# Optimization experiments

Measured on AMD Instinct MI355X. Metric: run time of the kernel, lower is better.

Reference implementation:

```python
import jax, jax.numpy as jnp
import numpy as np

PAD = 0

def setup_inputs() -> dict:
    key = jax.random.key(0)
    ks = jax.random.split(key, 16)
    B, S, D, F = 64, 512, 768, 256
    VOCAB = 32000
    # variable-length tweets: length in [8, S], rest is padding (token id PAD=0)
    lengths = jax.random.randint(ks[0], (B,), 8, S + 1)
    tok = jax.random.randint(ks[1], (B, S), 1, VOCAB)
    x = jnp.where(jnp.arange(S)[None, :] < lengths[:, None], tok, PAD)
    h = jax.random.normal(ks[2], (B, S, D), dtype=jnp.float32)
    sc = 0.02
    w2 = jax.random.normal(ks[3], (F, D, 2), dtype=jnp.float32) * sc
    b2 = jax.random.normal(ks[4], (F,), dtype=jnp.float32) * sc
    w3 = jax.random.normal(ks[5], (F, D, 3), dtype=jnp.float32) * sc
    b3 = jax.random.normal(ks[6], (F,), dtype=jnp.float32) * sc
    w4 = jax.random.normal(ks[7], (F, D, 4), dtype=jnp.float32) * sc
    b4 = jax.random.normal(ks[8], (F,), dtype=jnp.float32) * sc
    w5 = jax.random.normal(ks[9], (F, D, 5), dtype=jnp.float32) * sc
    b5 = jax.random.normal(ks[10], (F,), dtype=jnp.float32) * sc
    fc_w = jax.random.normal(ks[11], (1, 4 * F), dtype=jnp.float32) * sc
    fc_b = jax.random.normal(ks[12], (1,), dtype=jnp.float32) * sc
    return {"x": x, "h": h, "w2": w2, "b2": b2, "w3": w3, "b3": b3,
            "w4": w4, "b4": b4, "w5": w5, "b5": b5, "fc_w": fc_w, "fc_b": fc_b}


def _branch(hc, L, w, b):
    # hc: [B, D, S] front-compacted hidden states; w: [F, D, k]
    k = w.shape[-1]
    out = jax.lax.conv_general_dilated(
        hc, w, window_strides=(1,), padding='VALID',
        dimension_numbers=('NCH', 'OIH', 'NCH')) + b[None, :, None]  # [B,F,S-k+1]
    T = out.shape[-1]
    # conv position t is valid iff t + k - 1 < L  <=>  t < L - k + 1
    valid = jnp.arange(T)[None, :] < (L - k + 1)[:, None]           # [B,T]
    neg = jnp.asarray(-jnp.inf, out.dtype)
    pooled = jnp.max(jnp.where(valid[:, None, :], out, neg), axis=-1)  # [B,F]
    return jax.nn.relu(pooled)


def reference(x, h, w2, b2, w3, b3, w4, b4, w5, b5, fc_w, fc_b):
    mask = x != PAD                                   # [B,S]
    L = mask.sum(axis=1)                              # [B]
    # stable compaction: move non-pad token hidden states to the front, order preserved
    order = jnp.argsort(jnp.logical_not(mask), axis=1, stable=True)   # [B,S]
    hc = jnp.take_along_axis(h, order[..., None], axis=1)             # [B,S,D]
    hc = hc.transpose(0, 2, 1)                                        # [B,D,S]
    feats = jnp.concatenate([
        _branch(hc, L, w2, b2),
        _branch(hc, L, w3, b3),
        _branch(hc, L, w4, b4),
        _branch(hc, L, w5, b5),
    ], axis=-1)                                       # [B, 4F]
    logits = feats @ fc_w.T + fc_b                    # [B,1]
    return jax.nn.sigmoid(logits).squeeze(-1)         # [B]
```

## Files before the change

### kernel.cpp

```cpp
#include <hip/hip_runtime.h>
#include <stdint.h>

#define Bn 64
#define Sn 512
#define SPn 520
#define Dn 768
#define JSTRIDE 196608
#define ABUF 16640
#define BSLOT 8192
#define QS_A 28.222222f
#define SAQ 0.035433072f

typedef int iv4 __attribute__((ext_vector_type(4)));

static __device__ __forceinline__ signed char q8(float f, float s) {
  float t = __builtin_rintf(f * s);
  t = fmaxf(-127.f, fminf(127.f, t));
  return (signed char)(int)t;
}

static __device__ __forceinline__ void gload16(const void* g, void* l) {
  __builtin_amdgcn_global_load_lds(
      (const __attribute__((address_space(1))) unsigned int*)g,
      (__attribute__((address_space(3))) unsigned int*)l, 16, 0, 0);
}

template<int N> __device__ __forceinline__ void waitv() {
  static_assert(N == 0 || N == 2 || N == 7, "");
  if constexpr (N == 0) asm volatile("s_waitcnt vmcnt(0)" ::: "memory");
  else if constexpr (N == 2) asm volatile("s_waitcnt vmcnt(2)" ::: "memory");
  else asm volatile("s_waitcnt vmcnt(7)" ::: "memory");
}

__global__ __launch_bounds__(256) void compact_kernel(
    const int* __restrict__ x, const float* __restrict__ h,
    signed char* __restrict__ hcq, int* __restrict__ Lout) {
  int b = blockIdx.x, rblk = blockIdx.y;
  __shared__ unsigned long long masks[8];
  __shared__ short sidx[Sn];
  int tid = threadIdx.x, lane = tid & 63, wv = tid >> 6;
  for (int c = wv; c < 8; c += 4) {
    bool pred = x[b * Sn + c * 64 + lane] != 0;
    unsigned long long m = __ballot(pred);
    if (lane == 0) masks[c] = m;
  }
  __syncthreads();
  int pref[9]; pref[0] = 0;
  #pragma unroll
  for (int c = 0; c < 8; ++c) pref[c + 1] = pref[c] + __popcll(masks[c]);
  int L = pref[8];
  for (int p = tid; p < Sn; p += 256) {
    int c = p >> 6, l = p & 63;
    unsigned long long m = masks[c];
    if ((m >> l) & 1ull)
      sidx[pref[c] + __popcll(m & ((1ull << l) - 1ull))] = (short)p;
  }
  if (rblk == 0 && tid == 0) Lout[b] = L;
  __syncthreads();
  int r0 = rblk * 65;
  for (int r = r0 + wv; r < r0 + 65; r += 4) {
    if (r < L) {
      signed char* dst = hcq + ((size_t)b * SPn + r) * Dn;
      const float* src = h + ((size_t)b * Sn + sidx[r]) * Dn;
      #pragma unroll
      for (int c = 0; c < 3; ++c) {
        int d = c * 256 + lane * 4;
        float4 v = *(const float4*)(src + d);
        char4 o = { q8(v.x, QS_A), q8(v.y, QS_A), q8(v.z, QS_A), q8(v.w, QS_A) };
        *(char4*)(dst + d) = o;
      }
    }
  }
}

__global__ __launch_bounds__(256) void plan_kernel(
    const int* __restrict__ Lbuf, int* __restrict__ plan, int* __restrict__ rowmap) {
  __shared__ int sOff[65];
  __shared__ int sL[64];
  int tid = threadIdx.x;
  if (tid < 64) {
    int L = Lbuf[tid];
    int SL = (L + 15) & ~15;
    int pre = SL;
    #pragma unroll
    for (int off = 1; off < 64; off <<= 1) {
      int y = __shfl_up(pre, off);
      if (tid >= off) pre += y;
    }
    sOff[tid] = pre - SL;
    sL[tid] = L;
    if (tid == 63) { sOff[64] = pre; plan[0] = (pre + 255) >> 8; }
  }
  __syncthreads();
  int M = sOff[64];
  for (int b = 0; b < 64; ++b) {
    int off = sOff[b], L = sL[b];
    int SL = (L + 15) & ~15;
    int enc = (b << 20) | (L << 10);
    for (int t = tid; t < SL; t += 256) rowmap[off + t] = enc | t;
  }
  for (int p = M + tid; p < M + 264; p += 256)
    rowmap[p] = 512;
}

__global__ __launch_bounds__(256) void wpack_kernel(
    const float* __restrict__ w2, const float* __restrict__ w3,
    const float* __restrict__ w4, const float* __restrict__ w5,
    signed char* __restrict__ wq, float* __restrict__ fscale) {
  __shared__ float sf[3840];
  __shared__ float smax[4];
  int bb = blockIdx.x;
  int br = bb >> 8, f = bb & 255, k = br + 2;
  const float* w = (br == 0) ? w2 : (br == 1) ? w3 : (br == 2) ? w4 : w5;
  int mBase = 256 * ((br * (br + 3)) >> 1);
  const float* src = w + (size_t)f * Dn * k;
  int n = Dn * k;
  int tid = threadIdx.x, lane = tid & 63, wv = tid >> 6;
  float mx = 0.f;
  for (int e = tid; e < n; e += 256) {
    float v = src[e];
    sf[e] = v;
    mx = fmaxf(mx, fabsf(v));
  }
  #pragma unroll
  for (int off = 32; off; off >>= 1) mx = fmaxf(mx, __shfl_xor(mx, off));
  if (lane == 0) smax[wv] = mx;
  __syncthreads();
  float M = fmaxf(fmaxf(smax[0], smax[1]), fmaxf(smax[2], smax[3]));
  M = fmaxf(M, 1e-30f);
  if (tid == 0) fscale[br * 256 + f] = M / 127.f;
  float qs = 127.f / M;
  for (int j = 0; j < k; ++j) {
    signed char* dst = wq + (size_t)(mBase + j * 256 + f) * Dn;
    for (int d = tid; d < Dn; d += 256) dst[d] = q8(sf[d * k + j], qs);
  }
}

static __device__ __forceinline__ void issueA(
    int d0i, char* sA, const char* const (&gA)[4], const char* gAt,
    int lane, int wvoff) {
  int aoff = (d0i + 1) * 64;
  char* nA = sA + ((d0i + 1) & 1) * ABUF;
  #pragma unroll
  for (int p = 0; p < 4; ++p) gload16(gA[p] + aoff, nA + p * 4096 + wvoff);
  if (lane < 16) gload16(gAt + aoff, nA + 16384);
}

template<int J, int W, int J2, int DADD, int DOA>
static __device__ __forceinline__ void conv_step(
    int d0i, int bsl0, char* sA, char* sB,
    const char* const (&gA)[4], const char* gAt, const char* gB0,
    int lane, int wv, int lrow, int lg, int wvoff, iv4 (&acc)[4][8]) {
  int sl = bsl0 + J;      sl  -= (sl  >= 3) ? 3 : 0; sl  -= (sl  >= 3) ? 3 : 0;
  int dsl = bsl0 + J + 2; dsl -= (dsl >= 3) ? 3 : 0; dsl -= (dsl >= 3) ? 3 : 0; dsl -= (dsl >= 3) ? 3 : 0;
  {
    int boff = J2 * JSTRIDE + (d0i + DADD) * 64;
    char* bdst = sB + dsl * BSLOT + wvoff;
    gload16(gB0 + boff, bdst);
    gload16(gB0 + 49152 + boff, bdst + 4096);
  }
  if constexpr (DOA) issueA(d0i, sA, gA, gAt, lane, wvoff);
  const char* curA = sA + (d0i & 1) * ABUF;
  const char* curB = sB + sl * BSLOT;
  iv4 Af[4], Bf[8];
  #pragma unroll
  for (int m = 0; m < 4; ++m) {
    int row = wv * 64 + m * 16 + lrow + J;
    Af[m] = *(const iv4*)(curA + row * 64 + ((lg ^ ((row >> 1) & 3)) << 4));
  }
  #pragma unroll
  for (int n = 0; n < 8; ++n) {
    int row = n * 16 + lrow;
    Bf[n] = *(const iv4*)(curB + row * 64 + ((lg ^ ((row >> 1) & 3)) << 4));
  }
  __builtin_amdgcn_s_setprio(1);
  #pragma unroll
  for (int n = 0; n < 8; ++n)
    #pragma unroll
    for (int m = 0; m < 4; ++m)
      acc[m][n] = __builtin_amdgcn_mfma_i32_16x16x64_i8(Af[m], Bf[n], acc[m][n], 0, 0, 0);
  __builtin_amdgcn_s_setprio(0);
  __builtin_amdgcn_sched_barrier(0);
  waitv<W>();
  __builtin_amdgcn_sched_barrier(0);
  __builtin_amdgcn_s_barrier();
  __builtin_amdgcn_sched_barrier(0);
}

#define SA bsl0, sA, sB, gA, gAt, gB0, lane, wv, lrow, lg, wvoff, acc

template<int KK>
static __device__ __forceinline__ void conv_loop(
    char* sA, char* sB, const char* const (&gA)[4], const char* gAt,
    const char* gB0,
    int lane, int wv, int lrow, int lg, int wvoff, iv4 (&acc)[4][8]) {
  #pragma unroll
  for (int p = 0; p < 4; ++p) gload16(gA[p], sA + p * 4096 + wvoff);
  if (lane < 16) gload16(gAt, sA + 16384);
  gload16(gB0, sB + wvoff);
  gload16(gB0 + 49152, sB + 4096 + wvoff);
  gload16(gB0 + JSTRIDE, sB + BSLOT + wvoff);
  gload16(gB0 + 49152 + JSTRIDE, sB + BSLOT + 4096 + wvoff);
  __builtin_amdgcn_sched_barrier(0);
  waitv<2>();
  __builtin_amdgcn_sched_barrier(0);
  __builtin_amdgcn_s_barrier();
  __builtin_amdgcn_sched_barrier(0);
  int bsl0 = 0;
  for (int d0i = 0; d0i < 11; ++d0i) {
    if constexpr (KK == 5) {
      conv_step<0,7,2,0,1>(d0i, SA);
      conv_step<1,7,3,0,0>(d0i, SA);
      conv_step<2,2,4,0,0>(d0i, SA);
      conv_step<3,2,0,1,0>(d0i, SA);
      conv_step<4,2,1,1,0>(d0i, SA);
    } else if constexpr (KK == 4) {
      conv_step<0,7,2,0,1>(d0i, SA);
      conv_step<1,7,3,0,0>(d0i, SA);
      conv_step<2,2,0,1,0>(d0i, SA);
      conv_step<3,2,1,1,0>(d0i, SA);
    } else if constexpr (KK == 3) {
      conv_step<0,7,2,0,1>(d0i, SA);
      conv_step<1,7,0,1,0>(d0i, SA);
      conv_step<2,2,1,1,0>(d0i, SA);
    } else {
      conv_step<0,7,0,1,1>(d0i, SA);
      conv_step<1,2,1,1,0>(d0i, SA);
    }
    bsl0 += KK; bsl0 -= (bsl0 >= 3) ? 3 : 0; bsl0 -= (bsl0 >= 3) ? 3 : 0;
  }
  if constexpr (KK == 5) {
    conv_step<0,2,2,0,0>(11, SA);
    conv_step<1,2,3,0,0>(11, SA);
    conv_step<2,2,4,0,0>(11, SA);
    conv_step<3,2,0,1,0>(11, SA);
    conv_step<4,2,1,1,0>(11, SA);
  } else if constexpr (KK == 4) {
    conv_step<0,2,2,0,0>(11, SA);
    conv_step<1,2,3,0,0>(11, SA);
    conv_step<2,2,0,1,0>(11, SA);
    conv_step<3,2,1,1,0>(11, SA);
  } else if constexpr (KK == 3) {
    conv_step<0,2,2,0,0>(11, SA);
    conv_step<1,2,0,1,0>(11, SA);
    conv_step<2,2,1,1,0>(11, SA);
  } else {
    conv_step<0,2,0,1,0>(11, SA);
    conv_step<1,2,1,1,0>(11, SA);
  }
  waitv<0>();
}

__global__ __launch_bounds__(256, 2) void conv_kernel(
    const signed char* __restrict__ hcq, const signed char* __restrict__ wq,
    const float* __restrict__ b2, const float* __restrict__ b3,
    const float* __restrict__ b4, const float* __restrict__ b5,
    const float* __restrict__ fscale,
    const int* __restrict__ plan, const int* __restrict__ rowmap,
    int* __restrict__ feats) {
  __shared__ char smem[2 * ABUF + 3 * BSLOT];
  char* sA = smem;
  char* sB = smem + 2 * ABUF;
  int idx = blockIdx.x;
  int xcd = idx & 7, s2 = idx >> 3;
  int sub = s2 & 7, tile = xcd + ((s2 >> 3) << 3);
  if (tile >= plan[0]) return;
  int br = 3 - (sub >> 1), ff = sub & 1, kk = br + 2;
  int mBase = 256 * ((br * (br + 3)) >> 1) + ff * 128;
  const float* bias = (br == 0) ? b2 : (br == 1) ? b3 : (br == 2) ? b4 : b5;
  int tid = threadIdx.x, lane = tid & 63, wv = tid >> 6;
  int lrow = lane & 15, lg = lane >> 4;
  int wvoff = wv * 1024;
  int P0 = tile << 8;

  const char* gA[4];
  #pragma unroll
  for (int p = 0; p < 4; ++p) {
    int c = p * 256 + tid;
    int row = c >> 2, sgp = c & 3;
    int rm = rowmap[P0 + row];
    int bb_ = rm >> 20, t = rm & 1023;
    int seg = sgp ^ ((row >> 1) & 3);
    gA[p] = (const char*)(hcq + ((size_t)(bb_ * SPn + t)) * Dn + seg * 16);
  }
  const char* gAt;
  {
    int l = lane & 15;
    int row = 256 + (l >> 2), sgp = l & 3;
    int rm = rowmap[P0 + row];
    int bb_ = rm >> 20, t = rm & 1023;
    int seg = sgp ^ ((row >> 1) & 3);
    gAt = (const char*)(hcq + ((size_t)(bb_ * SPn + t)) * Dn + seg * 16);
  }
  const char* gB0;
  {
    int row = tid >> 2, sgp = tid & 3;
    int seg = sgp ^ ((row >> 1) & 3);
    gB0 = (const char*)(wq + ((size_t)(mBase + row)) * Dn + seg * 16);
  }

  iv4 acc[4][8];
  #pragma unroll
  for (int m = 0; m < 4; ++m)
    #pragma unroll
    for (int n = 0; n < 8; ++n) acc[m][n] = (iv4)0;

  switch (br) {
    case 3: conv_loop<5>(sA, sB, gA, gAt, gB0, lane, wv, lrow, lg, wvoff, acc); break;
    case 2: conv_loop<4>(sA, sB, gA, gAt, gB0, lane, wv, lrow, lg, wvoff, acc); break;
    case 1: conv_loop<3>(sA, sB, gA, gAt, gB0, lane, wv, lrow, lg, wvoff, acc); break;
    default: conv_loop<2>(sA, sB, gA, gAt, gB0, lane, wv, lrow, lg, wvoff, acc); break;
  }

  int rmv[4];
  #pragma unroll
  for (int m = 0; m < 4; ++m) rmv[m] = rowmap[P0 + wv * 64 + m * 16];
  #pragma unroll
  for (int n = 0; n < 8; ++n) {
    int fg = ff * 128 + n * 16 + lrow;
    float bv = bias[fg];
    float sfc = fscale[br * 256 + fg] * SAQ;
    #pragma unroll
    for (int m = 0; m < 4; ++m) {
      int bb_ = rmv[m] >> 20;
      int Lb = (rmv[m] >> 10) & 1023;
      int t0 = (rmv[m] & 1023) + lg * 4;
      int vlim = Lb - kk + 1;
      float pmax = 0.f;
      #pragma unroll
      for (int i = 0; i < 4; ++i) {
        float v = (float)acc[m][n][i] * sfc + bv;
        pmax = fmaxf(pmax, (t0 + i < vlim) ? fmaxf(v, 0.f) : 0.f);
      }
      pmax = fmaxf(pmax, __shfl_xor(pmax, 16));
      pmax = fmaxf(pmax, __shfl_xor(pmax, 32));
      if (lane < 16 && pmax > 0.f)
        atomicMax(feats + bb_ * 1024 + br * 256 + fg, __float_as_int(pmax));
    }
  }
}

__global__ __launch_bounds__(64) void fc_kernel(
    const int* __restrict__ feats, const float* __restrict__ fcw,
    const float* __restrict__ fcb, float* __restrict__ out) {
  int b = blockIdx.x, lane = threadIdx.x;
  float acc = 0.f;
  for (int i = lane; i < 1024; i += 64)
    acc += __int_as_float(feats[b * 1024 + i]) * fcw[i];
  #pragma unroll
  for (int off = 32; off; off >>= 1) acc += __shfl_xor(acc, off);
  if (lane == 0) out[b] = 1.f / (1.f + expf(-(acc + fcb[0])));
}

extern "C" void kernel_launch(void* const* d_in, const int* in_sizes, int n_in,
                              void* d_out, int out_size, void* d_ws, size_t ws_size,
                              hipStream_t stream) {
  const int*   x   = (const int*)d_in[0];
  const float* h   = (const float*)d_in[1];
  const float* w2  = (const float*)d_in[2];
  const float* b2  = (const float*)d_in[3];
  const float* w3  = (const float*)d_in[4];
  const float* b3  = (const float*)d_in[5];
  const float* w4  = (const float*)d_in[6];
  const float* b4  = (const float*)d_in[7];
  const float* w5  = (const float*)d_in[8];
  const float* b5  = (const float*)d_in[9];
  const float* fcw = (const float*)d_in[10];
  const float* fcb = (const float*)d_in[11];
  float* out = (float*)d_out;
  char* ws = (char*)d_ws;
  signed char* hcq = (signed char*)ws;
  signed char* wq  = (signed char*)(ws + 25559040);
  float* fscale = (float*)(ws + 28311552);
  int* feats  = (int*)(ws + 28315648);
  int* Lbuf   = (int*)(ws + 28577792);
  int* plan   = (int*)(ws + 28578048);
  int* rowmap = (int*)(ws + 28578064);

  hipMemsetAsync(feats, 0, 64 * 1024 * 4, stream);
  compact_kernel<<<dim3(64, 8), 256, 0, stream>>>(x, h, hcq, Lbuf);
  plan_kernel<<<1, 256, 0, stream>>>(Lbuf, plan, rowmap);
  wpack_kernel<<<1024, 256, 0, stream>>>(w2, w3, w4, w5, wq, fscale);
  conv_kernel<<<1024, 256, 0, stream>>>(hcq, wq, b2, b3, b4, b5, fscale, plan, rowmap, feats);
  fc_kernel<<<64, 64, 0, stream>>>(feats, fcw, fcb, out);
}
```

Before: 115.8 us.

## Fuse compaction and weight packing into one launch; split conv tile over 8 waves

Merges the compaction and weight-quantization kernels into a single stage kernel with 1536 blocks. The plan kernel now computes lengths directly from the token ids, so it no longer depends on compaction. The conv kernel moves from 4 waves with 64x128 per-wave tiles to 8 waves in a 4x2 grid with 64x64 per-wave tiles. This halves accumulator registers and global loads per thread, and the launch bounds are raised to target more occupancy. The cost is more LDS fragment reads per MFMA and barriers shared across more waves.

```diff
diff --git a/kernel.cpp b/kernel.cpp
--- a/kernel.cpp
+++ b/kernel.cpp
@@ -26,60 +26,28 @@
 }
 
 template<int N> __device__ __forceinline__ void waitv() {
-  static_assert(N == 0 || N == 2 || N == 7, "");
+  static_assert(N == 0 || N == 1 || N == 4, "");
   if constexpr (N == 0) asm volatile("s_waitcnt vmcnt(0)" ::: "memory");
-  else if constexpr (N == 2) asm volatile("s_waitcnt vmcnt(2)" ::: "memory");
-  else asm volatile("s_waitcnt vmcnt(7)" ::: "memory");
-}
-
-__global__ __launch_bounds__(256) void compact_kernel(
-    const int* __restrict__ x, const float* __restrict__ h,
-    signed char* __restrict__ hcq, int* __restrict__ Lout) {
-  int b = blockIdx.x, rblk = blockIdx.y;
-  __shared__ unsigned long long masks[8];
-  __shared__ short sidx[Sn];
+  else if constexpr (N == 1) asm volatile("s_waitcnt vmcnt(1)" ::: "memory");
+  else asm volatile("s_waitcnt vmcnt(4)" ::: "memory");
+}
+
+__global__ __launch_bounds__(256) void plan_kernel(
+    const int* __restrict__ x, int* __restrict__ plan, int* __restrict__ rowmap) {
+  __shared__ int sL[64];
+  __shared__ int sOff[65];
   int tid = threadIdx.x, lane = tid & 63, wv = tid >> 6;
-  for (int c = wv; c < 8; c += 4) {
-    bool pred = x[b * Sn + c * 64 + lane] != 0;
-    unsigned long long m = __ballot(pred);
-    if (lane == 0) masks[c] = m;
+  for (int bb = wv; bb < 64; bb += 4) {
+    int cnt = 0;
+    for (int c = 0; c < 8; ++c) {
+      unsigned long long m = __ballot(x[bb * Sn + c * 64 + lane] != 0);
+      cnt += __popcll(m);
+    }
+    if (lane == 0) sL[bb] = cnt;
   }
   __syncthreads();
-  int pref[9]; pref[0] = 0;
-  #pragma unroll
-  for (int c = 0; c < 8; ++c) pref[c + 1] = pref[c] + __popcll(masks[c]);
-  int L = pref[8];
-  for (int p = tid; p < Sn; p += 256) {
-    int c = p >> 6, l = p & 63;
-    unsigned long long m = masks[c];
-    if ((m >> l) & 1ull)
-      sidx[pref[c] + __popcll(m & ((1ull << l) - 1ull))] = (short)p;
-  }
-  if (rblk == 0 && tid == 0) Lout[b] = L;
-  __syncthreads();
-  int r0 = rblk * 65;
-  for (int r = r0 + wv; r < r0 + 65; r += 4) {
-    if (r < L) {
-      signed char* dst = hcq + ((size_t)b * SPn + r) * Dn;
-      const float* src = h + ((size_t)b * Sn + sidx[r]) * Dn;
-      #pragma unroll
-      for (int c = 0; c < 3; ++c) {
-        int d = c * 256 + lane * 4;
-        float4 v = *(const float4*)(src + d);
-        char4 o = { q8(v.x, QS_A), q8(v.y, QS_A), q8(v.z, QS_A), q8(v.w, QS_A) };
-        *(char4*)(dst + d) = o;
-      }
-    }
-  }
-}
-
-__global__ __launch_bounds__(256) void plan_kernel(
-    const int* __restrict__ Lbuf, int* __restrict__ plan, int* __restrict__ rowmap) {
-  __shared__ int sOff[65];
-  __shared__ int sL[64];
-  int tid = threadIdx.x;
   if (tid < 64) {
-    int L = Lbuf[tid];
+    int L = sL[tid];
     int SL = (L + 15) & ~15;
     int pre = SL;
     #pragma unroll
@@ -88,7 +56,6 @@
       if (tid >= off) pre += y;
     }
     sOff[tid] = pre - SL;
-    sL[tid] = L;
     if (tid == 63) { sOff[64] = pre; plan[0] = (pre + 255) >> 8; }
   }
   __syncthreads();
@@ -103,79 +70,116 @@
     rowmap[p] = 512;
 }
 
-__global__ __launch_bounds__(256) void wpack_kernel(
+__global__ __launch_bounds__(256) void stage_kernel(
+    const int* __restrict__ x, const float* __restrict__ h,
     const float* __restrict__ w2, const float* __restrict__ w3,
     const float* __restrict__ w4, const float* __restrict__ w5,
-    signed char* __restrict__ wq, float* __restrict__ fscale) {
-  __shared__ float sf[3840];
-  __shared__ float smax[4];
-  int bb = blockIdx.x;
-  int br = bb >> 8, f = bb & 255, k = br + 2;
-  const float* w = (br == 0) ? w2 : (br == 1) ? w3 : (br == 2) ? w4 : w5;
-  int mBase = 256 * ((br * (br + 3)) >> 1);
-  const float* src = w + (size_t)f * Dn * k;
-  int n = Dn * k;
+    signed char* __restrict__ hcq, signed char* __restrict__ wq,
+    float* __restrict__ fscale) {
   int tid = threadIdx.x, lane = tid & 63, wv = tid >> 6;
-  float mx = 0.f;
-  for (int e = tid; e < n; e += 256) {
-    float v = src[e];
-    sf[e] = v;
-    mx = fmaxf(mx, fabsf(v));
-  }
-  #pragma unroll
-  for (int off = 32; off; off >>= 1) mx = fmaxf(mx, __shfl_xor(mx, off));
-  if (lane == 0) smax[wv] = mx;
-  __syncthreads();
-  float M = fmaxf(fmaxf(smax[0], smax[1]), fmaxf(smax[2], smax[3]));
-  M = fmaxf(M, 1e-30f);
-  if (tid == 0) fscale[br * 256 + f] = M / 127.f;
-  float qs = 127.f / M;
-  for (int j = 0; j < k; ++j) {
-    signed char* dst = wq + (size_t)(mBase + j * 256 + f) * Dn;
-    for (int d = tid; d < Dn; d += 256) dst[d] = q8(sf[d * k + j], qs);
+  if (blockIdx.x < 512) {
+    int cidx = blockIdx.x;
+    int b = cidx >> 3, rblk = cidx & 7;
+    __shared__ unsigned long long masks[8];
+    __shared__ short sidx[Sn];
+    for (int c = wv; c < 8; c += 4) {
+      unsigned long long m = __ballot(x[b * Sn + c * 64 + lane] != 0);
+      if (lane == 0) masks[c] = m;
+    }
+    __syncthreads();
+    int pref[9]; pref[0] = 0;
+    #pragma unroll
+    for (int c = 0; c < 8; ++c) pref[c + 1] = pref[c] + __popcll(masks[c]);
+    int L = pref[8];
+    for (int p = tid; p < Sn; p += 256) {
+      int c = p >> 6, l = p & 63;
+      unsigned long long m = masks[c];
+      if ((m >> l) & 1ull)
+        sidx[pref[c] + __popcll(m & ((1ull << l) - 1ull))] = (short)p;
+    }
+    __syncthreads();
+    int r0 = rblk * 65;
+    for (int r = r0 + wv; r < r0 + 65; r += 4) {
+      if (r < L) {
+        signed char* dst = hcq + ((size_t)b * SPn + r) * Dn;
+        const float* src = h + ((size_t)b * Sn + sidx[r]) * Dn;
+        #pragma unroll
+        for (int c = 0; c < 3; ++c) {
+          int d = c * 256 + lane * 4;
+          float4 v = *(const float4*)(src + d);
+          char4 o = { q8(v.x, QS_A), q8(v.y, QS_A), q8(v.z, QS_A), q8(v.w, QS_A) };
+          *(char4*)(dst + d) = o;
+        }
+      }
+    }
+  } else {
+    __shared__ float sf[3840];
+    __shared__ float smax[4];
+    int bb = blockIdx.x - 512;
+    int br = bb >> 8, f = bb & 255, k = br + 2;
+    const float* w = (br == 0) ? w2 : (br == 1) ? w3 : (br == 2) ? w4 : w5;
+    int mBase = 256 * ((br * (br + 3)) >> 1);
+    const float* src = w + (size_t)f * Dn * k;
+    int n = Dn * k;
+    float mx = 0.f;
+    for (int e = tid; e < n; e += 256) {
+      float v = src[e];
+      sf[e] = v;
+      mx = fmaxf(mx, fabsf(v));
+    }
+    #pragma unroll
+    for (int off = 32; off; off >>= 1) mx = fmaxf(mx, __shfl_xor(mx, off));
+    if (lane == 0) smax[wv] = mx;
+    __syncthreads();
+    float M = fmaxf(fmaxf(smax[0], smax[1]), fmaxf(smax[2], smax[3]));
+    M = fmaxf(M, 1e-30f);
+    if (tid == 0) fscale[br * 256 + f] = M / 127.f;
+    float qs = 127.f / M;
+    for (int j = 0; j < k; ++j) {
+      signed char* dst = wq + (size_t)(mBase + j * 256 + f) * Dn;
+      for (int d = tid; d < Dn; d += 256) dst[d] = q8(sf[d * k + j], qs);
+    }
   }
 }
 
 static __device__ __forceinline__ void issueA(
-    int d0i, char* sA, const char* const (&gA)[4], const char* gAt,
+    int d0i, char* sA, const char* const (&gA)[2], const char* gAt,
     int lane, int wvoff) {
   int aoff = (d0i + 1) * 64;
   char* nA = sA + ((d0i + 1) & 1) * ABUF;
   #pragma unroll
-  for (int p = 0; p < 4; ++p) gload16(gA[p] + aoff, nA + p * 4096 + wvoff);
+  for (int p = 0; p < 2; ++p) gload16(gA[p] + aoff, nA + p * 8192 + wvoff);
   if (lane < 16) gload16(gAt + aoff, nA + 16384);
 }
 
 template<int J, int W, int J2, int DADD, int DOA>
 static __device__ __forceinline__ void conv_step(
     int d0i, int bsl0, char* sA, char* sB,
-    const char* const (&gA)[4], const char* gAt, const char* gB0,
-    int lane, int wv, int lrow, int lg, int wvoff, iv4 (&acc)[4][8]) {
+    const char* const (&gA)[2], const char* gAt, const char* gB0,
+    int lane, int wr, int wc, int lrow, int lg, int wvoff, iv4 (&acc)[4][4]) {
   int sl = bsl0 + J;      sl  -= (sl  >= 3) ? 3 : 0; sl  -= (sl  >= 3) ? 3 : 0;
-  int dsl = bsl0 + J + 2; dsl -= (dsl >= 3) ? 3 : 0; dsl -= (dsl >= 3) ? 3 : 0; dsl -= (dsl >= 3) ? 3 : 0;
+  int dsl = bsl0 + J + 2; dsl -= (dsl >= 3) ? 3 : 0; dsl -= (dsl >= 3) ? 3 : 0;
   {
     int boff = J2 * JSTRIDE + (d0i + DADD) * 64;
-    char* bdst = sB + dsl * BSLOT + wvoff;
-    gload16(gB0 + boff, bdst);
-    gload16(gB0 + 49152 + boff, bdst + 4096);
+    gload16(gB0 + boff, sB + dsl * BSLOT + wvoff);
   }
   if constexpr (DOA) issueA(d0i, sA, gA, gAt, lane, wvoff);
   const char* curA = sA + (d0i & 1) * ABUF;
   const char* curB = sB + sl * BSLOT;
-  iv4 Af[4], Bf[8];
+  iv4 Af[4], Bf[4];
   #pragma unroll
   for (int m = 0; m < 4; ++m) {
-    int row = wv * 64 + m * 16 + lrow + J;
+    int row = wr * 64 + m * 16 + lrow + J;
     Af[m] = *(const iv4*)(curA + row * 64 + ((lg ^ ((row >> 1) & 3)) << 4));
   }
   #pragma unroll
-  for (int n = 0; n < 8; ++n) {
-    int row = n * 16 + lrow;
+  for (int n = 0; n < 4; ++n) {
+    int row = wc * 64 + n * 16 + lrow;
     Bf[n] = *(const iv4*)(curB + row * 64 + ((lg ^ ((row >> 1) & 3)) << 4));
   }
   __builtin_amdgcn_s_setprio(1);
   #pragma unroll
-  for (int n = 0; n < 8; ++n)
+  for (int n = 0; n < 4; ++n)
     #pragma unroll
     for (int m = 0; m < 4; ++m)
       acc[m][n] = __builtin_amdgcn_mfma_i32_16x16x64_i8(Af[m], Bf[n], acc[m][n], 0, 0, 0);
@@ -187,71 +191,69 @@
   __builtin_amdgcn_sched_barrier(0);
 }
 
-#define SA bsl0, sA, sB, gA, gAt, gB0, lane, wv, lrow, lg, wvoff, acc
+#define SA bsl0, sA, sB, gA, gAt, gB0, lane, wr, wc, lrow, lg, wvoff, acc
 
 template<int KK>
 static __device__ __forceinline__ void conv_loop(
-    char* sA, char* sB, const char* const (&gA)[4], const char* gAt,
+    char* sA, char* sB, const char* const (&gA)[2], const char* gAt,
     const char* gB0,
-    int lane, int wv, int lrow, int lg, int wvoff, iv4 (&acc)[4][8]) {
-  #pragma unroll
-  for (int p = 0; p < 4; ++p) gload16(gA[p], sA + p * 4096 + wvoff);
+    int lane, int wr, int wc, int lrow, int lg, int wvoff, iv4 (&acc)[4][4]) {
+  #pragma unroll
+  for (int p = 0; p < 2; ++p) gload16(gA[p], sA + p * 8192 + wvoff);
   if (lane < 16) gload16(gAt, sA + 16384);
   gload16(gB0, sB + wvoff);
-  gload16(gB0 + 49152, sB + 4096 + wvoff);
   gload16(gB0 + JSTRIDE, sB + BSLOT + wvoff);
-  gload16(gB0 + 49152 + JSTRIDE, sB + BSLOT + 4096 + wvoff);
-  __builtin_amdgcn_sched_barrier(0);
-  waitv<2>();
+  __builtin_amdgcn_sched_barrier(0);
+  waitv<1>();
   __builtin_amdgcn_sched_barrier(0);
   __builtin_amdgcn_s_barrier();
   __builtin_amdgcn_sched_barrier(0);
   int bsl0 = 0;
   for (int d0i = 0; d0i < 11; ++d0i) {
     if constexpr (KK == 5) {
-      conv_step<0,7,2,0,1>(d0i, SA);
-      conv_step<1,7,3,0,0>(d0i, SA);
-      conv_step<2,2,4,0,0>(d0i, SA);
-      conv_step<3,2,0,1,0>(d0i, SA);
-      conv_step<4,2,1,1,0>(d0i, SA);
+      conv_step<0,4,2,0,1>(d0i, SA);
+      conv_step<1,4,3,0,0>(d0i, SA);
+      conv_step<2,1,4,0,0>(d0i, SA);
+      conv_step<3,1,0,1,0>(d0i, SA);
+      conv_step<4,1,1,1,0>(d0i, SA);
     } else if constexpr (KK == 4) {
-      conv_step<0,7,2,0,1>(d0i, SA);
-      conv_step<1,7,3,0,0>(d0i, SA);
-      conv_step<2,2,0,1,0>(d0i, SA);
-      conv_step<3,2,1,1,0>(d0i, SA);
+      conv_step<0,4,2,0,1>(d0i, SA);
+      conv_step<1,4,3,0,0>(d0i, SA);
+      conv_step<2,1,0,1,0>(d0i, SA);
+      conv_step<3,1,1,1,0>(d0i, SA);
     } else if constexpr (KK == 3) {
-      conv_step<0,7,2,0,1>(d0i, SA);
-      conv_step<1,7,0,1,0>(d0i, SA);
-      conv_step<2,2,1,1,0>(d0i, SA);
+      conv_step<0,4,2,0,1>(d0i, SA);
+      conv_step<1,4,0,1,0>(d0i, SA);
+      conv_step<2,1,1,1,0>(d0i, SA);
     } else {
-      conv_step<0,7,0,1,1>(d0i, SA);
-      conv_step<1,2,1,1,0>(d0i, SA);
+      conv_step<0,4,0,1,1>(d0i, SA);
+      conv_step<1,1,1,1,0>(d0i, SA);
     }
     bsl0 += KK; bsl0 -= (bsl0 >= 3) ? 3 : 0; bsl0 -= (bsl0 >= 3) ? 3 : 0;
   }
   if constexpr (KK == 5) {
-    conv_step<0,2,2,0,0>(11, SA);
-    conv_step<1,2,3,0,0>(11, SA);
-    conv_step<2,2,4,0,0>(11, SA);
-    conv_step<3,2,0,1,0>(11, SA);
-    conv_step<4,2,1,1,0>(11, SA);
+    conv_step<0,1,2,0,0>(11, SA);
+    conv_step<1,1,3,0,0>(11, SA);
+    conv_step<2,1,4,0,0>(11, SA);
+    conv_step<3,1,0,1,0>(11, SA);
+    conv_step<4,1,1,1,0>(11, SA);
   } else if constexpr (KK == 4) {
-    conv_step<0,2,2,0,0>(11, SA);
-    conv_step<1,2,3,0,0>(11, SA);
-    conv_step<2,2,0,1,0>(11, SA);
-    conv_step<3,2,1,1,0>(11, SA);
+    conv_step<0,1,2,0,0>(11, SA);
+    conv_step<1,1,3,0,0>(11, SA);
+    conv_step<2,1,0,1,0>(11, SA);
+    conv_step<3,1,1,1,0>(11, SA);
   } else if constexpr (KK == 3) {
-    conv_step<0,2,2,0,0>(11, SA);
-    conv_step<1,2,0,1,0>(11, SA);
-    conv_step<2,2,1,1,0>(11, SA);
+    conv_step<0,1,2,0,0>(11, SA);
+    conv_step<1,1,0,1,0>(11, SA);
+    conv_step<2,1,1,1,0>(11, SA);
   } else {
-    conv_step<0,2,0,1,0>(11, SA);
-    conv_step<1,2,1,1,0>(11, SA);
+    conv_step<0,1,0,1,0>(11, SA);
+    conv_step<1,1,1,1,0>(11, SA);
   }
   waitv<0>();
 }
 
-__global__ __launch_bounds__(256, 2) void conv_kernel(
+__global__ __launch_bounds__(512, 4) void conv_kernel(
     const signed char* __restrict__ hcq, const signed char* __restrict__ wq,
     const float* __restrict__ b2, const float* __restrict__ b3,
     const float* __restrict__ b4, const float* __restrict__ b5,
@@ -269,14 +271,15 @@
   int mBase = 256 * ((br * (br + 3)) >> 1) + ff * 128;
   const float* bias = (br == 0) ? b2 : (br == 1) ? b3 : (br == 2) ? b4 : b5;
   int tid = threadIdx.x, lane = tid & 63, wv = tid >> 6;
+  int wr = wv >> 1, wc = wv & 1;
   int lrow = lane & 15, lg = lane >> 4;
   int wvoff = wv * 1024;
   int P0 = tile << 8;
 
-  const char* gA[4];
-  #pragma unroll
-  for (int p = 0; p < 4; ++p) {
-    int c = p * 256 + tid;
+  const char* gA[2];
+  #pragma unroll
+  for (int p = 0; p < 2; ++p) {
+    int c = p * 512 + tid;
     int row = c >> 2, sgp = c & 3;
     int rm = rowmap[P0 + row];
     int bb_ = rm >> 20, t = rm & 1023;
@@ -299,25 +302,25 @@
     gB0 = (const char*)(wq + ((size_t)(mBase + row)) * Dn + seg * 16);
   }
 
-  iv4 acc[4][8];
+  iv4 acc[4][4];
   #pragma unroll
   for (int m = 0; m < 4; ++m)
     #pragma unroll
-    for (int n = 0; n < 8; ++n) acc[m][n] = (iv4)0;
+    for (int n = 0; n < 4; ++n) acc[m][n] = (iv4)0;
 
   switch (br) {
-    case 3: conv_loop<5>(sA, sB, gA, gAt, gB0, lane, wv, lrow, lg, wvoff, acc); break;
-    case 2: conv_loop<4>(sA, sB, gA, gAt, gB0, lane, wv, lrow, lg, wvoff, acc); break;
-    case 1: conv_loop<3>(sA, sB, gA, gAt, gB0, lane, wv, lrow, lg, wvoff, acc); break;
-    default: conv_loop<2>(sA, sB, gA, gAt, gB0, lane, wv, lrow, lg, wvoff, acc); break;
+    case 3: conv_loop<5>(sA, sB, gA, gAt, gB0, lane, wr, wc, lrow, lg, wvoff, acc); break;
+    case 2: conv_loop<4>(sA, sB, gA, gAt, gB0, lane, wr, wc, lrow, lg, wvoff, acc); break;
+    case 1: conv_loop<3>(sA, sB, gA, gAt, gB0, lane, wr, wc, lrow, lg, wvoff, acc); break;
+    default: conv_loop<2>(sA, sB, gA, gAt, gB0, lane, wr, wc, lrow, lg, wvoff, acc); break;
   }
 
   int rmv[4];
   #pragma unroll
-  for (int m = 0; m < 4; ++m) rmv[m] = rowmap[P0 + wv * 64 + m * 16];
-  #pragma unroll
-  for (int n = 0; n < 8; ++n) {
-    int fg = ff * 128 + n * 16 + lrow;
+  for (int m = 0; m < 4; ++m) rmv[m] = rowmap[P0 + wr * 64 + m * 16];
+  #pragma unroll
+  for (int n = 0; n < 4; ++n) {
+    int fg = ff * 128 + wc * 64 + n * 16 + lrow;
     float bv = bias[fg];
     float sfc = fscale[br * 256 + fg] * SAQ;
     #pragma unroll
@@ -373,14 +376,12 @@
   signed char* wq  = (signed char*)(ws + 25559040);
   float* fscale = (float*)(ws + 28311552);
   int* feats  = (int*)(ws + 28315648);
-  int* Lbuf   = (int*)(ws + 28577792);
-  int* plan   = (int*)(ws + 28578048);
-  int* rowmap = (int*)(ws + 28578064);
+  int* plan   = (int*)(ws + 28577792);
+  int* rowmap = (int*)(ws + 28577808);
 
   hipMemsetAsync(feats, 0, 64 * 1024 * 4, stream);
-  compact_kernel<<<dim3(64, 8), 256, 0, stream>>>(x, h, hcq, Lbuf);
-  plan_kernel<<<1, 256, 0, stream>>>(Lbuf, plan, rowmap);
-  wpack_kernel<<<1024, 256, 0, stream>>>(w2, w3, w4, w5, wq, fscale);
-  conv_kernel<<<1024, 256, 0, stream>>>(hcq, wq, b2, b3, b4, b5, fscale, plan, rowmap, feats);
+  plan_kernel<<<1, 256, 0, stream>>>(x, plan, rowmap);
+  stage_kernel<<<1536, 256, 0, stream>>>(x, h, w2, w3, w4, w5, hcq, wq, fscale);
+  conv_kernel<<<1024, 512, 0, stream>>>(hcq, wq, b2, b3, b4, b5, fscale, plan, rowmap, feats);
   fc_kernel<<<64, 64, 0, stream>>>(feats, fcw, fcb, out);
 }
```

After: 115.2 us. Within noise of the previous version (-0.6%).
